# Kernel tuning notes

Hardware: AMD Instinct MI355X
Metric: run time of the kernel (lower is better)

The kernel has to match this reference:

```python
import jax, jax.numpy as jnp
import numpy as np

N, T, D, H = 32, 1024, 512, 512


def setup_inputs() -> dict:
    key = jax.random.key(0)
    k1, k2, k3, k4 = jax.random.split(key, 4)
    x = jax.random.normal(k1, (N, T, D), dtype=jnp.float32)
    h0 = jax.random.normal(k2, (N, H), dtype=jnp.float32)
    Wx = jax.random.normal(k3, (D, 4 * H), dtype=jnp.float32) / np.sqrt(D)
    Wh = jax.random.normal(k4, (H, 4 * H), dtype=jnp.float32) / np.sqrt(H)
    b = jnp.zeros((4 * H,), dtype=jnp.float32)
    return {"x": x, "h0": h0, "Wx": Wx, "Wh": Wh, "b": b}


def reference(x, h0, Wx, Wh, b):
    Hdim = h0.shape[1]
    # Precompute input projection for all timesteps: (N,T,4H)
    xW = jnp.einsum('ntd,dk->ntk', x, Wx) + b

    def step(carry, xw_t):
        h, c = carry
        a = xw_t + h @ Wh  # (N,4H)
        i = jax.nn.sigmoid(a[:, :Hdim])
        f = jax.nn.sigmoid(a[:, Hdim:2 * Hdim])
        o = jax.nn.sigmoid(a[:, 2 * Hdim:3 * Hdim])
        g = jnp.tanh(a[:, 3 * Hdim:])
        c_next = f * c + i * g
        h_next = o * jnp.tanh(c_next)
        return (h_next, c_next), h_next

    c0 = jnp.zeros_like(h0)
    xW_t = jnp.swapaxes(xW, 0, 1)  # (T,N,4H) for scan over time
    _, hs = jax.lax.scan(step, (h0, c0), xW_t)
    return jnp.swapaxes(hs, 0, 1)  # (N,T,H)
```

## Files before the change

kernel.cpp:

```cpp
#include <hip/hip_runtime.h>
#include <hip/hip_bf16.h>


#define NWG 32
#define TOTAL_WG 256
#define LDW 520
#define SMEM_BYTES (2*64*LDW*2 + 4*32*16*4 + 512*4)

typedef __attribute__((ext_vector_type(8))) short s16x8;
typedef __attribute__((ext_vector_type(4))) float f32x4;
typedef __attribute__((ext_vector_type(4))) float f4v;

__device__ __forceinline__ float b2f(unsigned short u) {
  unsigned v = ((unsigned)u) << 16;
  return __builtin_bit_cast(float, v);
}
__device__ __forceinline__ unsigned short f2b(float f) {
  unsigned u = __builtin_bit_cast(unsigned, f);
  unsigned r = (u + 0x7fffu + ((u >> 16) & 1u)) >> 16;
  return (unsigned short)r;
}
__device__ __forceinline__ float sigmoidf_(float x) {
  return 1.f / (1.f + __expf(-x));
}
__device__ __forceinline__ float tanhf_(float x) {
  float ax = fabsf(x);
  float e = __expf(-2.f * ax);
  float th = (1.f - e) / (1.f + e);
  return copysignf(th, x);
}

__device__ __forceinline__ void burn(float& a, float& b) {
#pragma unroll
  for (int i = 0; i < 64; i++) {
    a = __builtin_fmaf(a, 1.0000002f, 1e-9f);
    b = __builtin_fmaf(b, 0.9999998f, 1e-9f);
  }
}

__device__ __forceinline__ void store_flag_l2(unsigned* p, unsigned v) {
  asm volatile("global_store_dword %0, %1, off sc0"
               :: "v"(p), "v"(v) : "memory");
}
__device__ __forceinline__ unsigned load_flag_l2(const unsigned* p) {
  unsigned r;
  asm volatile("global_load_dword %0, %1, off sc0\n\t"
               "s_waitcnt vmcnt(0)"
               : "=v"(r) : "v"(p) : "memory");
  return r;
}
__device__ __forceinline__ void store_dword_dev(unsigned* p, unsigned v) {
  asm volatile("global_store_dword %0, %1, off sc0 sc1"
               :: "v"(p), "v"(v) : "memory");
}
__device__ __forceinline__ unsigned load_dword_dev(const unsigned* p) {
  unsigned r;
  asm volatile("global_load_dword %0, %1, off sc0 sc1\n\t"
               "s_waitcnt vmcnt(0)"
               : "=v"(r) : "v"(p) : "memory");
  return r;
}

__device__ __forceinline__ void split8(const float* p, s16x8& hi, s16x8& lo) {
  float tmp[8];
  *(f4v*)&tmp[0] = *(const f4v*)&p[0];
  *(f4v*)&tmp[4] = *(const f4v*)&p[4];
#pragma unroll
  for (int j = 0; j < 8; j++) {
    unsigned short h = f2b(tmp[j]);
    hi[j] = (short)h;
    lo[j] = (short)f2b(tmp[j] - b2f(h));
  }
}
__device__ __forceinline__ s16x8 cvt8(const float* p) {
  float tmp[8];
  *(f4v*)&tmp[0] = *(const f4v*)&p[0];
  *(f4v*)&tmp[4] = *(const f4v*)&p[4];
  s16x8 r;
#pragma unroll
  for (int j = 0; j < 8; j++) r[j] = (short)f2b(tmp[j]);
  return r;
}

__device__ __forceinline__ bool sniff_is_bf16(const unsigned short* wx) {
  int cnt = 0;
  for (int i = 0; i < 512; i++) {
    unsigned e = (wx[i] >> 7) & 0xFF;
    cnt += (e >= 0x60 && e <= 0x9F) ? 1 : 0;
  }
  return cnt >= 440;
}

template <bool F32>
__device__ __forceinline__ void lstm_body(
    const void* xv, const void* h0v, const void* Wxv, const void* Whv,
    const void* biasv, void* outv, unsigned* __restrict__ bar,
    unsigned char* smem, int w) {
  unsigned short* WhS = (unsigned short*)smem;
  unsigned short* WxS = (unsigned short*)(smem + 64 * LDW * 2);
  float* gatebuf = (float*)(smem + 2 * 64 * LDW * 2);
  float* cbuf = (float*)(smem + 2 * 64 * LDW * 2 + 4 * 32 * 16 * 4);

  const unsigned short* xb = (const unsigned short*)xv;
  const float* xf = (const float*)xv;
  const unsigned short* h0b = (const unsigned short*)h0v;
  const float* h0f = (const float*)h0v;

  const int tid = threadIdx.x;
  const int g = tid >> 6;
  const int lane = tid & 63;
  const int lm = lane & 15;
  const int q = lane >> 4;

  float bu0 = 1.0f, bu1 = 1.0f;

  for (int i = 0; i < 8; i++) {
    int id = tid + i * 256;
    int gate = id & 3;
    int k = id >> 2;
    size_t base = (size_t)k * 2048 + gate * 512 + w * 16;
    if (F32) {
      const float* px = (const float*)Wxv + base;
      const float* ph = (const float*)Whv + base;
#pragma unroll
      for (int seg = 0; seg < 4; seg++) {
        f4v vx = *(const f4v*)(px + seg * 4);
        f4v vh = *(const f4v*)(ph + seg * 4);
#pragma unroll
        for (int j = 0; j < 4; j++) {
          WxS[(gate * 16 + seg * 4 + j) * LDW + k] = f2b(vx[j]);
          WhS[(gate * 16 + seg * 4 + j) * LDW + k] = f2b(vh[j]);
        }
      }
    } else {
      const unsigned short* px = (const unsigned short*)Wxv + base;
      const unsigned short* ph = (const unsigned short*)Whv + base;
      s16x8 vx0 = *(const s16x8*)&px[0];
      s16x8 vx1 = *(const s16x8*)&px[8];
      s16x8 vh0 = *(const s16x8*)&ph[0];
      s16x8 vh1 = *(const s16x8*)&ph[8];
#pragma unroll
      for (int j = 0; j < 8; j++) {
        WxS[(gate * 16 + j) * LDW + k]     = (unsigned short)vx0[j];
        WxS[(gate * 16 + 8 + j) * LDW + k] = (unsigned short)vx1[j];
        WhS[(gate * 16 + j) * LDW + k]     = (unsigned short)vh0[j];
        WhS[(gate * 16 + 8 + j) * LDW + k] = (unsigned short)vh1[j];
      }
    }
  }
  cbuf[tid] = 0.f;
  cbuf[tid + 256] = 0.f;

  float bv[2][4];
  for (int pp = 0; pp < 2; pp++) {
    int p = tid + pp * 256;
    int j = p & 15;
    for (int qq = 0; qq < 4; qq++) {
      int idx = qq * 512 + w * 16 + j;
      bv[pp][qq] = F32 ? ((const float*)biasv)[idx]
                       : b2f(((const unsigned short*)biasv)[idx]);
    }
  }
  __syncthreads();

  for (int t = 0; t < 1024; t++) {
    f32x4 acc0 = {0.f, 0.f, 0.f, 0.f};
    f32x4 acc1 = {0.f, 0.f, 0.f, 0.f};

    if (F32) {
      for (int kc = 0; kc < 16; kc++) {
        int k = kc * 32 + q * 8;
        s16x8 bfrag = *(const s16x8*)&WxS[(g * 16 + lm) * LDW + k];
        s16x8 a0 = cvt8(&xf[(size_t)(lm * 1024 + t) * 512 + k]);
        s16x8 a1 = cvt8(&xf[(size_t)((16 + lm) * 1024 + t) * 512 + k]);
        acc0 = __builtin_amdgcn_mfma_f32_16x16x32_bf16(a0, bfrag, acc0, 0, 0, 0);
        acc1 = __builtin_amdgcn_mfma_f32_16x16x32_bf16(a1, bfrag, acc1, 0, 0, 0);
      }
    } else {
      for (int kc = 0; kc < 16; kc++) {
        int k = kc * 32 + q * 8;
        s16x8 bfrag = *(const s16x8*)&WxS[(g * 16 + lm) * LDW + k];
        s16x8 a0 = *(const s16x8*)&xb[(size_t)(lm * 1024 + t) * 512 + k];
        s16x8 a1 = *(const s16x8*)&xb[(size_t)((16 + lm) * 1024 + t) * 512 + k];
        acc0 = __builtin_amdgcn_mfma_f32_16x16x32_bf16(a0, bfrag, acc0, 0, 0, 0);
        acc1 = __builtin_amdgcn_mfma_f32_16x16x32_bf16(a1, bfrag, acc1, 0, 0, 0);
      }
    }

    if (t > 0) {
      const unsigned target = (unsigned)t;
      const unsigned* fp = bar + (lane & 31);
      int guard = 0;
      for (;;) {
        unsigned v = load_flag_l2(fp);
        if (__all(v >= target)) break;
        burn(bu0, bu1);
        if (++guard > (1 << 22)) break;
      }
      asm volatile("buffer_inv" ::: "memory");
    }

    if (F32) {
      float* outf = (float*)outv;
      const float* hpf = (t == 0) ? h0f : outf + (size_t)(t - 1) * 512;
      const size_t hstride = (t == 0) ? 512 : (size_t)1024 * 512;
      for (int kc = 0; kc < 16; kc++) {
        int k = kc * 32 + q * 8;
        s16x8 bfrag = *(const s16x8*)&WhS[(g * 16 + lm) * LDW + k];
        s16x8 hi0, lo0, hi1, lo1;
        split8(&hpf[lm * hstride + k], hi0, lo0);
        split8(&hpf[(16 + lm) * hstride + k], hi1, lo1);
        acc0 = __builtin_amdgcn_mfma_f32_16x16x32_bf16(hi0, bfrag, acc0, 0, 0, 0);
        acc0 = __builtin_amdgcn_mfma_f32_16x16x32_bf16(lo0, bfrag, acc0, 0, 0, 0);
        acc1 = __builtin_amdgcn_mfma_f32_16x16x32_bf16(hi1, bfrag, acc1, 0, 0, 0);
        acc1 = __builtin_amdgcn_mfma_f32_16x16x32_bf16(lo1, bfrag, acc1, 0, 0, 0);
      }
    } else {
      unsigned short* outb = (unsigned short*)outv;
      const unsigned short* hpb = (t == 0) ? h0b : outb + (size_t)(t - 1) * 512;
      const size_t hstride = (t == 0) ? 512 : (size_t)1024 * 512;
      for (int kc = 0; kc < 16; kc++) {
        int k = kc * 32 + q * 8;
        s16x8 bfrag = *(const s16x8*)&WhS[(g * 16 + lm) * LDW + k];
        s16x8 a0 = *(const s16x8*)&hpb[lm * hstride + k];
        s16x8 a1 = *(const s16x8*)&hpb[(16 + lm) * hstride + k];
        acc0 = __builtin_amdgcn_mfma_f32_16x16x32_bf16(a0, bfrag, acc0, 0, 0, 0);
        acc1 = __builtin_amdgcn_mfma_f32_16x16x32_bf16(a1, bfrag, acc1, 0, 0, 0);
      }
    }

    for (int r = 0; r < 4; r++) {
      gatebuf[(g * 32 + q * 4 + r) * 16 + lm] = acc0[r];
      gatebuf[(g * 32 + 16 + q * 4 + r) * 16 + lm] = acc1[r];
    }
    __syncthreads();

    for (int pp = 0; pp < 2; pp++) {
      int p = tid + pp * 256;
      int n = p >> 4, j = p & 15;
      float ai = gatebuf[(0 * 32 + n) * 16 + j] + bv[pp][0];
      float af = gatebuf[(1 * 32 + n) * 16 + j] + bv[pp][1];
      float ao = gatebuf[(2 * 32 + n) * 16 + j] + bv[pp][2];
      float ag = gatebuf[(3 * 32 + n) * 16 + j] + bv[pp][3];
      float iG = sigmoidf_(ai);
      float fG = sigmoidf_(af);
      float oG = sigmoidf_(ao);
      float gG = tanhf_(ag);
      float c = fG * cbuf[p] + iG * gG;
      cbuf[p] = c;
      float h = oG * tanhf_(c);
      size_t oidx = (size_t)(n * 1024 + t) * 512 + w * 16 + j;
      if (F32) ((float*)outv)[oidx] = h;
      else     ((unsigned short*)outv)[oidx] = f2b(h);
    }
    asm volatile("s_waitcnt vmcnt(0)" ::: "memory");
    __syncthreads();

    if (t < 1023 && tid == 0) {
      store_flag_l2(bar + w, (unsigned)(t + 1));
    }
  }
  asm volatile("" :: "v"(bu0), "v"(bu1));
}

__global__ __launch_bounds__(256) void lstm_kernel(
    const void* x, const void* h0, const void* Wx, const void* Wh,
    const void* bias, void* out, unsigned* ws) {
  extern __shared__ unsigned char smem[];
  __shared__ unsigned s_role[2];
  unsigned* flags  = ws;
  unsigned* cnt    = ws + 32;
  unsigned* winner = ws + 48;
  unsigned* done   = ws + 49;

  if (threadIdx.x == 0) {
    unsigned xcd;
    asm volatile("s_getreg_b32 %0, hwreg(HW_REG_XCC_ID)" : "=s"(xcd));
    xcd &= 0xFu;
    unsigned rank = atomicAdd(&cnt[xcd], 1u);
    if (rank == 31u) atomicCAS(winner, 0u, xcd + 1u);
    unsigned wv; int guard = 0;
    do {
      wv = load_dword_dev(winner);
    } while (wv == 0u && ++guard < (1 << 26));
    s_role[0] = (wv == xcd + 1u && rank < 32u) ? 1u : 0u;
    s_role[1] = rank;
  }
  __syncthreads();

  if (s_role[0]) {
    int w = (int)s_role[1];
    if (sniff_is_bf16((const unsigned short*)Wx))
      lstm_body<false>(x, h0, Wx, Wh, bias, out, flags, smem, w);
    else
      lstm_body<true>(x, h0, Wx, Wh, bias, out, flags, smem, w);
    if (w == 0 && threadIdx.x == 0) store_dword_dev(done, 1u);
  } else {
    float a = 1.0f;
    const float bm = 1.0000001f;
    for (int o = 0; o < (1 << 22); ++o) {
#pragma unroll
      for (int i = 0; i < 64; i++) a = __builtin_fmaf(a, bm, 1e-7f);
      __builtin_amdgcn_s_sleep(2);
      if ((o & 63) == 0) {
        if (load_dword_dev(done) != 0u) break;
      }
    }
    asm volatile("" :: "v"(a));
  }
}

extern "C" void kernel_launch(void* const* d_in, const int* in_sizes, int n_in,
                              void* d_out, int out_size, void* d_ws, size_t ws_size,
                              hipStream_t stream) {
  const void* x  = d_in[0];
  const void* h0 = d_in[1];
  const void* Wx = d_in[2];
  const void* Wh = d_in[3];
  const void* b  = d_in[4];
  void* out = d_out;
  unsigned* ws = (unsigned*)d_ws;

  hipMemsetAsync(ws, 0, 256, stream);

  hipFuncSetAttribute((const void*)lstm_kernel,
                      hipFuncAttributeMaxDynamicSharedMemorySize, SMEM_BYTES);

  void* args[] = {(void*)&x, (void*)&h0, (void*)&Wx, (void*)&Wh,
                  (void*)&b, (void*)&out, (void*)&ws};
  hipLaunchCooperativeKernel((const void*)lstm_kernel, dim3(TOTAL_WG), dim3(256),
                             args, SMEM_BYTES, stream);
}
```

Measured before the change: 25.16 ms.

## Precompute input projection across all workgroups before the recurrent phase

```diff
diff --git a/kernel.cpp b/kernel.cpp
--- a/kernel.cpp
+++ b/kernel.cpp
@@ -6,6 +6,7 @@
 #define TOTAL_WG 256
 #define LDW 520
 #define SMEM_BYTES (2*64*LDW*2 + 4*32*16*4 + 512*4)
+#define XW_BYTES (268435456ULL)
 
 typedef __attribute__((ext_vector_type(8))) short s16x8;
 typedef __attribute__((ext_vector_type(4))) float f32x4;
@@ -53,6 +54,11 @@
   asm volatile("global_store_dword %0, %1, off sc0 sc1"
                :: "v"(p), "v"(v) : "memory");
 }
+__device__ __forceinline__ void store_f32_dev(float* p, float v) {
+  unsigned u = __builtin_bit_cast(unsigned, v);
+  asm volatile("global_store_dword %0, %1, off sc0 sc1"
+               :: "v"(p), "v"(u) : "memory");
+}
 __device__ __forceinline__ unsigned load_dword_dev(const unsigned* p) {
   unsigned r;
   asm volatile("global_load_dword %0, %1, off sc0 sc1\n\t"
@@ -91,20 +97,65 @@
   return cnt >= 440;
 }
 
-template <bool F32>
-__device__ __forceinline__ void lstm_body(
+__device__ __forceinline__ void xw_phase(
+    const unsigned short* xb, const unsigned short* Wxv,
+    float* __restrict__ xwbuf, unsigned char* smem, int bid, int tid) {
+  unsigned short* WxS = (unsigned short*)(smem + 64 * LDW * 2);
+  const int w2 = bid & 31;
+  const int tc = bid >> 5;
+  for (int i = 0; i < 8; i++) {
+    int id = tid + i * 256;
+    int gate = id & 3;
+    int k = id >> 2;
+    const unsigned short* px = Wxv + (size_t)k * 2048 + gate * 512 + w2 * 16;
+    s16x8 v0 = *(const s16x8*)&px[0];
+    s16x8 v1 = *(const s16x8*)&px[8];
+#pragma unroll
+    for (int j = 0; j < 8; j++) {
+      WxS[(gate * 16 + j) * LDW + k]     = (unsigned short)v0[j];
+      WxS[(gate * 16 + 8 + j) * LDW + k] = (unsigned short)v1[j];
+    }
+  }
+  __syncthreads();
+
+  const int g = tid >> 6;
+  const int lane = tid & 63;
+  const int lm = lane & 15;
+  const int q = lane >> 4;
+
+  for (int t = tc * 128; t < tc * 128 + 128; t++) {
+    f32x4 acc0 = {0.f, 0.f, 0.f, 0.f};
+    f32x4 acc1 = {0.f, 0.f, 0.f, 0.f};
+    for (int kc = 0; kc < 16; kc++) {
+      int k = kc * 32 + q * 8;
+      s16x8 bfrag = *(const s16x8*)&WxS[(g * 16 + lm) * LDW + k];
+      s16x8 a0 = *(const s16x8*)&xb[(size_t)(lm * 1024 + t) * 512 + k];
+      s16x8 a1 = *(const s16x8*)&xb[(size_t)((16 + lm) * 1024 + t) * 512 + k];
+      acc0 = __builtin_amdgcn_mfma_f32_16x16x32_bf16(a0, bfrag, acc0, 0, 0, 0);
+      acc1 = __builtin_amdgcn_mfma_f32_16x16x32_bf16(a1, bfrag, acc1, 0, 0, 0);
+    }
+    float* bp = xwbuf + (size_t)t * 65536 + g * 512 + w2 * 16 + lm;
+#pragma unroll
+    for (int r = 0; r < 4; r++) {
+      store_f32_dev(bp + (size_t)(q * 4 + r) * 2048, acc0[r]);
+      store_f32_dev(bp + (size_t)(16 + q * 4 + r) * 2048, acc1[r]);
+    }
+  }
+  asm volatile("s_waitcnt vmcnt(0)" ::: "memory");
+}
+
+__device__ __forceinline__ void lstm_body_bf16(
     const void* xv, const void* h0v, const void* Wxv, const void* Whv,
     const void* biasv, void* outv, unsigned* __restrict__ bar,
-    unsigned char* smem, int w) {
+    const float* __restrict__ xwbuf, unsigned char* smem, int w) {
   unsigned short* WhS = (unsigned short*)smem;
   unsigned short* WxS = (unsigned short*)(smem + 64 * LDW * 2);
   float* gatebuf = (float*)(smem + 2 * 64 * LDW * 2);
   float* cbuf = (float*)(smem + 2 * 64 * LDW * 2 + 4 * 32 * 16 * 4);
 
   const unsigned short* xb = (const unsigned short*)xv;
-  const float* xf = (const float*)xv;
   const unsigned short* h0b = (const unsigned short*)h0v;
-  const float* h0f = (const float*)h0v;
+  unsigned short* outb = (unsigned short*)outv;
 
   const int tid = threadIdx.x;
   const int g = tid >> 6;
@@ -119,33 +170,18 @@
     int gate = id & 3;
     int k = id >> 2;
     size_t base = (size_t)k * 2048 + gate * 512 + w * 16;
-    if (F32) {
-      const float* px = (const float*)Wxv + base;
-      const float* ph = (const float*)Whv + base;
-#pragma unroll
-      for (int seg = 0; seg < 4; seg++) {
-        f4v vx = *(const f4v*)(px + seg * 4);
-        f4v vh = *(const f4v*)(ph + seg * 4);
-#pragma unroll
-        for (int j = 0; j < 4; j++) {
-          WxS[(gate * 16 + seg * 4 + j) * LDW + k] = f2b(vx[j]);
-          WhS[(gate * 16 + seg * 4 + j) * LDW + k] = f2b(vh[j]);
-        }
-      }
-    } else {
-      const unsigned short* px = (const unsigned short*)Wxv + base;
-      const unsigned short* ph = (const unsigned short*)Whv + base;
-      s16x8 vx0 = *(const s16x8*)&px[0];
-      s16x8 vx1 = *(const s16x8*)&px[8];
-      s16x8 vh0 = *(const s16x8*)&ph[0];
-      s16x8 vh1 = *(const s16x8*)&ph[8];
-#pragma unroll
-      for (int j = 0; j < 8; j++) {
-        WxS[(gate * 16 + j) * LDW + k]     = (unsigned short)vx0[j];
-        WxS[(gate * 16 + 8 + j) * LDW + k] = (unsigned short)vx1[j];
-        WhS[(gate * 16 + j) * LDW + k]     = (unsigned short)vh0[j];
-        WhS[(gate * 16 + 8 + j) * LDW + k] = (unsigned short)vh1[j];
-      }
+    const unsigned short* px = (const unsigned short*)Wxv + base;
+    const unsigned short* ph = (const unsigned short*)Whv + base;
+    s16x8 vx0 = *(const s16x8*)&px[0];
+    s16x8 vx1 = *(const s16x8*)&px[8];
+    s16x8 vh0 = *(const s16x8*)&ph[0];
+    s16x8 vh1 = *(const s16x8*)&ph[8];
+#pragma unroll
+    for (int j = 0; j < 8; j++) {
+      WxS[(gate * 16 + j) * LDW + k]     = (unsigned short)vx0[j];
+      WxS[(gate * 16 + 8 + j) * LDW + k] = (unsigned short)vx1[j];
+      WhS[(gate * 16 + j) * LDW + k]     = (unsigned short)vh0[j];
+      WhS[(gate * 16 + 8 + j) * LDW + k] = (unsigned short)vh1[j];
     }
   }
   cbuf[tid] = 0.f;
@@ -155,26 +191,37 @@
   for (int pp = 0; pp < 2; pp++) {
     int p = tid + pp * 256;
     int j = p & 15;
-    for (int qq = 0; qq < 4; qq++) {
-      int idx = qq * 512 + w * 16 + j;
-      bv[pp][qq] = F32 ? ((const float*)biasv)[idx]
-                       : b2f(((const unsigned short*)biasv)[idx]);
-    }
+    for (int qq = 0; qq < 4; qq++)
+      bv[pp][qq] = b2f(((const unsigned short*)biasv)[qq * 512 + w * 16 + j]);
   }
   __syncthreads();
+
+  if (xwbuf) {
+    if (tid == 0) {
+      const unsigned* p1 = bar + 50;
+      int guard = 0;
+      while (load_dword_dev(p1) < (unsigned)TOTAL_WG) {
+        __builtin_amdgcn_s_sleep(2);
+        if (++guard > (1 << 24)) break;
+      }
+    }
+    __syncthreads();
+  }
 
   for (int t = 0; t < 1024; t++) {
     f32x4 acc0 = {0.f, 0.f, 0.f, 0.f};
     f32x4 acc1 = {0.f, 0.f, 0.f, 0.f};
-
-    if (F32) {
-      for (int kc = 0; kc < 16; kc++) {
-        int k = kc * 32 + q * 8;
-        s16x8 bfrag = *(const s16x8*)&WxS[(g * 16 + lm) * LDW + k];
-        s16x8 a0 = cvt8(&xf[(size_t)(lm * 1024 + t) * 512 + k]);
-        s16x8 a1 = cvt8(&xf[(size_t)((16 + lm) * 1024 + t) * 512 + k]);
-        acc0 = __builtin_amdgcn_mfma_f32_16x16x32_bf16(a0, bfrag, acc0, 0, 0, 0);
-        acc1 = __builtin_amdgcn_mfma_f32_16x16x32_bf16(a1, bfrag, acc1, 0, 0, 0);
+    float xwv[2][4];
+
+    if (xwbuf) {
+      const float* xt = xwbuf + (size_t)t * 65536 + w * 16;
+#pragma unroll
+      for (int pp = 0; pp < 2; pp++) {
+        int p = tid + pp * 256;
+        int n = p >> 4, j = p & 15;
+#pragma unroll
+        for (int qq = 0; qq < 4; qq++)
+          xwv[pp][qq] = xt[(size_t)n * 2048 + qq * 512 + j];
       }
     } else {
       for (int kc = 0; kc < 16; kc++) {
@@ -185,6 +232,8 @@
         acc0 = __builtin_amdgcn_mfma_f32_16x16x32_bf16(a0, bfrag, acc0, 0, 0, 0);
         acc1 = __builtin_amdgcn_mfma_f32_16x16x32_bf16(a1, bfrag, acc1, 0, 0, 0);
       }
+      xwv[0][0] = xwv[0][1] = xwv[0][2] = xwv[0][3] = 0.f;
+      xwv[1][0] = xwv[1][1] = xwv[1][2] = xwv[1][3] = 0.f;
     }
 
     if (t > 0) {
@@ -200,7 +249,129 @@
       asm volatile("buffer_inv" ::: "memory");
     }
 
-    if (F32) {
+    {
+      const unsigned short* hpb = (t == 0) ? h0b : outb + (size_t)(t - 1) * 512;
+      const size_t hstride = (t == 0) ? 512 : (size_t)1024 * 512;
+      for (int kc = 0; kc < 16; kc++) {
+        int k = kc * 32 + q * 8;
+        s16x8 bfrag = *(const s16x8*)&WhS[(g * 16 + lm) * LDW + k];
+        s16x8 a0 = *(const s16x8*)&hpb[lm * hstride + k];
+        s16x8 a1 = *(const s16x8*)&hpb[(16 + lm) * hstride + k];
+        acc0 = __builtin_amdgcn_mfma_f32_16x16x32_bf16(a0, bfrag, acc0, 0, 0, 0);
+        acc1 = __builtin_amdgcn_mfma_f32_16x16x32_bf16(a1, bfrag, acc1, 0, 0, 0);
+      }
+    }
+
+    for (int r = 0; r < 4; r++) {
+      gatebuf[(g * 32 + q * 4 + r) * 16 + lm] = acc0[r];
+      gatebuf[(g * 32 + 16 + q * 4 + r) * 16 + lm] = acc1[r];
+    }
+    __syncthreads();
+
+    for (int pp = 0; pp < 2; pp++) {
+      int p = tid + pp * 256;
+      int n = p >> 4, j = p & 15;
+      float ai = gatebuf[(0 * 32 + n) * 16 + j] + xwv[pp][0] + bv[pp][0];
+      float af = gatebuf[(1 * 32 + n) * 16 + j] + xwv[pp][1] + bv[pp][1];
+      float ao = gatebuf[(2 * 32 + n) * 16 + j] + xwv[pp][2] + bv[pp][2];
+      float ag = gatebuf[(3 * 32 + n) * 16 + j] + xwv[pp][3] + bv[pp][3];
+      float iG = sigmoidf_(ai);
+      float fG = sigmoidf_(af);
+      float oG = sigmoidf_(ao);
+      float gG = tanhf_(ag);
+      float c = fG * cbuf[p] + iG * gG;
+      cbuf[p] = c;
+      float h = oG * tanhf_(c);
+      size_t oidx = (size_t)(n * 1024 + t) * 512 + w * 16 + j;
+      outb[oidx] = f2b(h);
+    }
+    asm volatile("s_waitcnt vmcnt(0)" ::: "memory");
+    __syncthreads();
+
+    if (t < 1023 && tid == 0) {
+      store_flag_l2(bar + w, (unsigned)(t + 1));
+    }
+  }
+  asm volatile("" :: "v"(bu0), "v"(bu1));
+}
+
+__device__ __forceinline__ void lstm_body_f32(
+    const void* xv, const void* h0v, const void* Wxv, const void* Whv,
+    const void* biasv, void* outv, unsigned* __restrict__ bar,
+    unsigned char* smem, int w) {
+  unsigned short* WhS = (unsigned short*)smem;
+  unsigned short* WxS = (unsigned short*)(smem + 64 * LDW * 2);
+  float* gatebuf = (float*)(smem + 2 * 64 * LDW * 2);
+  float* cbuf = (float*)(smem + 2 * 64 * LDW * 2 + 4 * 32 * 16 * 4);
+
+  const float* xf = (const float*)xv;
+  const float* h0f = (const float*)h0v;
+
+  const int tid = threadIdx.x;
+  const int g = tid >> 6;
+  const int lane = tid & 63;
+  const int lm = lane & 15;
+  const int q = lane >> 4;
+
+  float bu0 = 1.0f, bu1 = 1.0f;
+
+  for (int i = 0; i < 8; i++) {
+    int id = tid + i * 256;
+    int gate = id & 3;
+    int k = id >> 2;
+    size_t base = (size_t)k * 2048 + gate * 512 + w * 16;
+    const float* px = (const float*)Wxv + base;
+    const float* ph = (const float*)Whv + base;
+#pragma unroll
+    for (int seg = 0; seg < 4; seg++) {
+      f4v vx = *(const f4v*)(px + seg * 4);
+      f4v vh = *(const f4v*)(ph + seg * 4);
+#pragma unroll
+      for (int j = 0; j < 4; j++) {
+        WxS[(gate * 16 + seg * 4 + j) * LDW + k] = f2b(vx[j]);
+        WhS[(gate * 16 + seg * 4 + j) * LDW + k] = f2b(vh[j]);
+      }
+    }
+  }
+  cbuf[tid] = 0.f;
+  cbuf[tid + 256] = 0.f;
+
+  float bv[2][4];
+  for (int pp = 0; pp < 2; pp++) {
+    int p = tid + pp * 256;
+    int j = p & 15;
+    for (int qq = 0; qq < 4; qq++)
+      bv[pp][qq] = ((const float*)biasv)[qq * 512 + w * 16 + j];
+  }
+  __syncthreads();
+
+  for (int t = 0; t < 1024; t++) {
+    f32x4 acc0 = {0.f, 0.f, 0.f, 0.f};
+    f32x4 acc1 = {0.f, 0.f, 0.f, 0.f};
+
+    for (int kc = 0; kc < 16; kc++) {
+      int k = kc * 32 + q * 8;
+      s16x8 bfrag = *(const s16x8*)&WxS[(g * 16 + lm) * LDW + k];
+      s16x8 a0 = cvt8(&xf[(size_t)(lm * 1024 + t) * 512 + k]);
+      s16x8 a1 = cvt8(&xf[(size_t)((16 + lm) * 1024 + t) * 512 + k]);
+      acc0 = __builtin_amdgcn_mfma_f32_16x16x32_bf16(a0, bfrag, acc0, 0, 0, 0);
+      acc1 = __builtin_amdgcn_mfma_f32_16x16x32_bf16(a1, bfrag, acc1, 0, 0, 0);
+    }
+
+    if (t > 0) {
+      const unsigned target = (unsigned)t;
+      const unsigned* fp = bar + (lane & 31);
+      int guard = 0;
+      for (;;) {
+        unsigned v = load_flag_l2(fp);
+        if (__all(v >= target)) break;
+        burn(bu0, bu1);
+        if (++guard > (1 << 22)) break;
+      }
+      asm volatile("buffer_inv" ::: "memory");
+    }
+
+    {
       float* outf = (float*)outv;
       const float* hpf = (t == 0) ? h0f : outf + (size_t)(t - 1) * 512;
       const size_t hstride = (t == 0) ? 512 : (size_t)1024 * 512;
@@ -214,18 +385,6 @@
         acc0 = __builtin_amdgcn_mfma_f32_16x16x32_bf16(lo0, bfrag, acc0, 0, 0, 0);
         acc1 = __builtin_amdgcn_mfma_f32_16x16x32_bf16(hi1, bfrag, acc1, 0, 0, 0);
         acc1 = __builtin_amdgcn_mfma_f32_16x16x32_bf16(lo1, bfrag, acc1, 0, 0, 0);
-      }
-    } else {
-      unsigned short* outb = (unsigned short*)outv;
-      const unsigned short* hpb = (t == 0) ? h0b : outb + (size_t)(t - 1) * 512;
-      const size_t hstride = (t == 0) ? 512 : (size_t)1024 * 512;
-      for (int kc = 0; kc < 16; kc++) {
-        int k = kc * 32 + q * 8;
-        s16x8 bfrag = *(const s16x8*)&WhS[(g * 16 + lm) * LDW + k];
-        s16x8 a0 = *(const s16x8*)&hpb[lm * hstride + k];
-        s16x8 a1 = *(const s16x8*)&hpb[(16 + lm) * hstride + k];
-        acc0 = __builtin_amdgcn_mfma_f32_16x16x32_bf16(a0, bfrag, acc0, 0, 0, 0);
-        acc1 = __builtin_amdgcn_mfma_f32_16x16x32_bf16(a1, bfrag, acc1, 0, 0, 0);
       }
     }
 
@@ -250,8 +409,7 @@
       cbuf[p] = c;
       float h = oG * tanhf_(c);
       size_t oidx = (size_t)(n * 1024 + t) * 512 + w * 16 + j;
-      if (F32) ((float*)outv)[oidx] = h;
-      else     ((unsigned short*)outv)[oidx] = f2b(h);
+      ((float*)outv)[oidx] = h;
     }
     asm volatile("s_waitcnt vmcnt(0)" ::: "memory");
     __syncthreads();
@@ -265,13 +423,14 @@
 
 __global__ __launch_bounds__(256) void lstm_kernel(
     const void* x, const void* h0, const void* Wx, const void* Wh,
-    const void* bias, void* out, unsigned* ws) {
+    const void* bias, void* out, unsigned* ws, float* xwbuf) {
   extern __shared__ unsigned char smem[];
   __shared__ unsigned s_role[2];
   unsigned* flags  = ws;
   unsigned* cnt    = ws + 32;
   unsigned* winner = ws + 48;
   unsigned* done   = ws + 49;
+  unsigned* p1cnt  = ws + 50;
 
   if (threadIdx.x == 0) {
     unsigned xcd;
@@ -288,12 +447,23 @@
   }
   __syncthreads();
 
+  bool isbf = sniff_is_bf16((const unsigned short*)Wx);
+
+  if (xwbuf != nullptr) {
+    if (isbf)
+      xw_phase((const unsigned short*)x, (const unsigned short*)Wx,
+               xwbuf, smem, (int)blockIdx.x, (int)threadIdx.x);
+    __syncthreads();
+    if (threadIdx.x == 0) atomicAdd(p1cnt, 1u);
+  }
+
   if (s_role[0]) {
     int w = (int)s_role[1];
-    if (sniff_is_bf16((const unsigned short*)Wx))
-      lstm_body<false>(x, h0, Wx, Wh, bias, out, flags, smem, w);
+    if (isbf)
+      lstm_body_bf16(x, h0, Wx, Wh, bias, out, flags,
+                     isbf ? xwbuf : nullptr, smem, w);
     else
-      lstm_body<true>(x, h0, Wx, Wh, bias, out, flags, smem, w);
+      lstm_body_f32(x, h0, Wx, Wh, bias, out, flags, smem, w);
     if (w == 0 && threadIdx.x == 0) store_dword_dev(done, 1u);
   } else {
     float a = 1.0f;
@@ -323,11 +493,15 @@
 
   hipMemsetAsync(ws, 0, 256, stream);
 
+  float* xwbuf = nullptr;
+  if (ws_size >= XW_BYTES + 4096)
+    xwbuf = (float*)((char*)d_ws + 4096);
+
   hipFuncSetAttribute((const void*)lstm_kernel,
                       hipFuncAttributeMaxDynamicSharedMemorySize, SMEM_BYTES);
 
   void* args[] = {(void*)&x, (void*)&h0, (void*)&Wx, (void*)&Wh,
-                  (void*)&b, (void*)&out, (void*)&ws};
+                  (void*)&b, (void*)&out, (void*)&ws, (void*)&xwbuf};
   hipLaunchCooperativeKernel((const void*)lstm_kernel, dim3(TOTAL_WG), dim3(256),
                              args, SMEM_BYTES, stream);
 }
```

Result: faster. 24.42 ms (-3.0%).
